# Optimization experiments

Hardware: AMD Instinct MI355X
Metric: run time of the kernel (lower is better)

Reference implementation:

```python
import jax, jax.numpy as jnp
import numpy as np

V_TH = 1.0       # v_threshold
INIT_TAU = 2.0   # raw tau; decay = sigmoid(INIT_TAU)
T, B, IN_SZ, OUT_SZ = 32, 128, 2048, 2048


def setup_inputs() -> dict:
    key = jax.random.key(0)
    k1, k2 = jax.random.split(key)
    x = jax.random.normal(k1, (T, B, IN_SZ), jnp.float32)
    kernel = jax.random.normal(k2, (IN_SZ, OUT_SZ), jnp.float32) / np.sqrt(IN_SZ)
    return {"x": x, "kernel": kernel}


def reference(x, kernel):
    """Forward of Approx_OTPE's inner SNN step (f), scanned over time and
    vmapped over batch. Cell: u' = sigmoid(init_tau)*u + x @ W;
    s = heaviside(u' - v_th); soft reset u_out = u' - s*v_th.
    Returns stacked spikes [T, B, OUT_SZ]."""
    sig_tau = jax.nn.sigmoid(jnp.asarray(INIT_TAU, x.dtype))
    _, batch, _ = x.shape
    out_sz = kernel.shape[1]
    u0 = jnp.zeros((batch, out_sz), x.dtype)

    def body(u, xt):
        u_next = sig_tau * u + xt @ kernel          # [B, O]
        s = (u_next >= V_TH).astype(x.dtype)        # spike_fn forward
        u_out = u_next - s * V_TH                   # soft reset
        return u_out, s

    _, spikes = jax.lax.scan(body, u0, x)
    return spikes
```

## Files before the change

kernel.cpp:

```cpp
#include <hip/hip_runtime.h>
#include <math.h>

constexpr int T_STEPS = 32;
constexpr int BATCH   = 128;
constexpr int IN_SZ   = 2048;
constexpr int OUT_SZ  = 2048;

__global__ __launch_bounds__(256, 1) void Approx_OTPE_67181878444197_kernel(
        const float* __restrict__ x,
        const float* __restrict__ W,
        float* __restrict__ out) {
    constexpr int BK = 32, BM = 128, BN = 64;
    constexpr int YSTR = BN + 1;
    constexpr int YSZ  = BM * YSTR;

    __shared__ float smem[YSZ];
    float* const As = smem;
    float* const Bs = smem + BK * BM;

    const int o0  = blockIdx.x * BN;
    const int b0  = blockIdx.y * 4;
    const int tid = threadIdx.x;
    const int ty  = tid >> 4;
    const int tx  = tid & 15;

    const int am = tid >> 1;
    const int ak = (tid & 1) * 16;
    const int at = am >> 2;
    const int ab = am & 3;
    const size_t aBase = ((size_t)at * BATCH + (size_t)(b0 + ab)) * IN_SZ + ak;

    const int br = tid >> 4;
    const int bc = (tid & 15) * 4;

    float acc[8][4] = {};
    float su[8][4]  = {};

    #pragma unroll 1
    for (int it = 0; it < IN_SZ / BK; ++it) {
        const int k0 = it * BK;
        const float4 a0 = *reinterpret_cast<const float4*>(&x[aBase + k0]);
        const float4 a1 = *reinterpret_cast<const float4*>(&x[aBase + k0 + 4]);
        const float4 a2 = *reinterpret_cast<const float4*>(&x[aBase + k0 + 8]);
        const float4 a3 = *reinterpret_cast<const float4*>(&x[aBase + k0 + 12]);
        const float4 v0 = *reinterpret_cast<const float4*>(
            &W[(size_t)(k0 + br) * OUT_SZ + o0 + bc]);
        const float4 v1 = *reinterpret_cast<const float4*>(
            &W[(size_t)(k0 + 16 + br) * OUT_SZ + o0 + bc]);

        if (it == 16 || it == 32 || it == 48) {
            #pragma unroll
            for (int i = 0; i < 8; ++i)
                #pragma unroll
                for (int j = 0; j < 4; ++j) {
                    su[i][j]  = __fadd_rn(su[i][j], acc[i][j]);
                    acc[i][j] = 0.0f;
                }
        }

        __syncthreads();
        As[(ak +  0) * BM + am] = a0.x;
        As[(ak +  1) * BM + am] = a0.y;
        As[(ak +  2) * BM + am] = a0.z;
        As[(ak +  3) * BM + am] = a0.w;
        As[(ak +  4) * BM + am] = a1.x;
        As[(ak +  5) * BM + am] = a1.y;
        As[(ak +  6) * BM + am] = a1.z;
        As[(ak +  7) * BM + am] = a1.w;
        As[(ak +  8) * BM + am] = a2.x;
        As[(ak +  9) * BM + am] = a2.y;
        As[(ak + 10) * BM + am] = a2.z;
        As[(ak + 11) * BM + am] = a2.w;
        As[(ak + 12) * BM + am] = a3.x;
        As[(ak + 13) * BM + am] = a3.y;
        As[(ak + 14) * BM + am] = a3.z;
        As[(ak + 15) * BM + am] = a3.w;
        *reinterpret_cast<float4*>(&Bs[br * BN + bc])        = v0;
        *reinterpret_cast<float4*>(&Bs[(br + 16) * BN + bc]) = v1;
        __syncthreads();

        #pragma unroll
        for (int k = 0; k < BK; ++k) {
            const float4 x0 = *reinterpret_cast<const float4*>(&As[k * BM + ty * 8]);
            const float4 x1 = *reinterpret_cast<const float4*>(&As[k * BM + ty * 8 + 4]);
            const float4 wf = *reinterpret_cast<const float4*>(&Bs[k * BN + tx * 4]);
            const float a[8] = {x0.x, x0.y, x0.z, x0.w, x1.x, x1.y, x1.z, x1.w};
            const float w[4] = {wf.x, wf.y, wf.z, wf.w};
            #pragma unroll
            for (int i = 0; i < 8; ++i)
                #pragma unroll
                for (int j = 0; j < 4; ++j)
                    acc[i][j] = __builtin_fmaf(a[i], w[j], acc[i][j]);
        }
    }

    __syncthreads();
    #pragma unroll
    for (int i = 0; i < 8; ++i)
        #pragma unroll
        for (int j = 0; j < 4; ++j)
            smem[(ty * 8 + i) * YSTR + tx * 4 + j] = __fadd_rn(su[i][j], acc[i][j]);
    __syncthreads();

    {
        const int bl = tid >> 6;
        const int o  = tid & 63;
        const size_t plane  = (size_t)BATCH * OUT_SZ;
        const size_t outIdx = (size_t)(b0 + bl) * OUT_SZ + o0 + o;

        const double D = 1.0 / (1.0 + exp(-2.0));
        double u = 0.0;
        #pragma unroll
        for (int t = 0; t < T_STEPS; ++t) {
            const double y  = (double)smem[(t * 4 + bl) * YSTR + o];
            const double un = __dadd_rn(__dmul_rn(D, u), y);
            const double s  = (un >= 1.0) ? 1.0 : 0.0;
            u = __dsub_rn(un, s);
            out[(size_t)t * plane + outIdx] = (float)s;
        }
    }
}

extern "C" void kernel_launch(void* const* d_in, const int* in_sizes, int n_in,
                              void* d_out, int out_size, void* d_ws, size_t ws_size,
                              hipStream_t stream) {
    const float* x = (const float*)d_in[0];
    const float* W = (const float*)d_in[1];
    float* out     = (float*)d_out;

    dim3 grid(OUT_SZ / 64, BATCH / 4);
    Approx_OTPE_67181878444197_kernel<<<grid, 256, 0, stream>>>(x, W, out);
}
```

Before: 464.2 us.

## Split-K GEMM into workspace partials then combine and scan in separate kernel

The fused GEMM+scan kernel is replaced, when workspace allows, by a split-K GEMM that writes four partial products over the full T*B row range into a workspace, followed by a kernel that sums the partials in fixed order and runs the spiking scan per (b,o). This gives four times more blocks and a contiguous M tiling to raise occupancy across CUs. In exchange it adds about 128 MB of workspace writes and reads plus a second launch. If the workspace is too small, the original fused kernel is kept as a fallback.

After: 435.3 us. 6.2% less time.

```diff
diff --git a/kernel.cpp b/kernel.cpp
--- a/kernel.cpp
+++ b/kernel.cpp
@@ -5,58 +5,46 @@
 constexpr int BATCH   = 128;
 constexpr int IN_SZ   = 2048;
 constexpr int OUT_SZ  = 2048;
+constexpr int M_ROWS  = T_STEPS * BATCH;
+
 
 __global__ __launch_bounds__(256, 1) void Approx_OTPE_67181878444197_kernel(
         const float* __restrict__ x,
         const float* __restrict__ W,
-        float* __restrict__ out) {
+        float* __restrict__ ws) {
     constexpr int BK = 32, BM = 128, BN = 64;
-    constexpr int YSTR = BN + 1;
-    constexpr int YSZ  = BM * YSTR;
-
-    __shared__ float smem[YSZ];
-    float* const As = smem;
-    float* const Bs = smem + BK * BM;
+
+    __shared__ float As[BK * BM];
+    __shared__ float Bs[BK * BN];
 
     const int o0  = blockIdx.x * BN;
-    const int b0  = blockIdx.y * 4;
+    const int m0  = blockIdx.y * BM;
+    const int z   = blockIdx.z;
+    const int kz  = z * 512;
     const int tid = threadIdx.x;
     const int ty  = tid >> 4;
     const int tx  = tid & 15;
 
     const int am = tid >> 1;
     const int ak = (tid & 1) * 16;
-    const int at = am >> 2;
-    const int ab = am & 3;
-    const size_t aBase = ((size_t)at * BATCH + (size_t)(b0 + ab)) * IN_SZ + ak;
+    const size_t aBase = (size_t)(m0 + am) * IN_SZ + kz + ak;
 
     const int br = tid >> 4;
     const int bc = (tid & 15) * 4;
 
     float acc[8][4] = {};
-    float su[8][4]  = {};
 
     #pragma unroll 1
-    for (int it = 0; it < IN_SZ / BK; ++it) {
+    for (int it = 0; it < 512 / BK; ++it) {
         const int k0 = it * BK;
         const float4 a0 = *reinterpret_cast<const float4*>(&x[aBase + k0]);
         const float4 a1 = *reinterpret_cast<const float4*>(&x[aBase + k0 + 4]);
         const float4 a2 = *reinterpret_cast<const float4*>(&x[aBase + k0 + 8]);
         const float4 a3 = *reinterpret_cast<const float4*>(&x[aBase + k0 + 12]);
         const float4 v0 = *reinterpret_cast<const float4*>(
-            &W[(size_t)(k0 + br) * OUT_SZ + o0 + bc]);
+            &W[(size_t)(kz + k0 + br) * OUT_SZ + o0 + bc]);
         const float4 v1 = *reinterpret_cast<const float4*>(
-            &W[(size_t)(k0 + 16 + br) * OUT_SZ + o0 + bc]);
-
-        if (it == 16 || it == 32 || it == 48) {
-            #pragma unroll
-            for (int i = 0; i < 8; ++i)
-                #pragma unroll
-                for (int j = 0; j < 4; ++j) {
-                    su[i][j]  = __fadd_rn(su[i][j], acc[i][j]);
-                    acc[i][j] = 0.0f;
-                }
-        }
+            &W[(size_t)(kz + k0 + 16 + br) * OUT_SZ + o0 + bc]);
 
         __syncthreads();
         As[(ak +  0) * BM + am] = a0.x;
@@ -94,6 +82,132 @@
         }
     }
 
+    float* const wz = ws + (size_t)z * M_ROWS * OUT_SZ;
+    #pragma unroll
+    for (int i = 0; i < 8; ++i) {
+        float4 v;
+        v.x = acc[i][0]; v.y = acc[i][1]; v.z = acc[i][2]; v.w = acc[i][3];
+        *reinterpret_cast<float4*>(
+            &wz[(size_t)(m0 + ty * 8 + i) * OUT_SZ + o0 + tx * 4]) = v;
+    }
+}
+
+__global__ __launch_bounds__(256, 1) void snn_combine_scan(
+        const float* __restrict__ ws, float* __restrict__ out) {
+    const int gid = blockIdx.x * 256 + threadIdx.x;
+    const int b   = gid >> 11;
+    const int o   = gid & 2047;
+    const size_t plane = (size_t)BATCH * OUT_SZ;
+    constexpr size_t ZS = (size_t)M_ROWS * OUT_SZ;
+
+    const double D = 1.0 / (1.0 + exp(-2.0));
+    double u = 0.0;
+    #pragma unroll 1
+    for (int t = 0; t < T_STEPS; ++t) {
+        const size_t r = (size_t)(t * BATCH + b) * OUT_SZ + o;
+        const float p0 = ws[r];
+        const float p1 = ws[r + ZS];
+        const float p2 = ws[r + 2 * ZS];
+        const float p3 = ws[r + 3 * ZS];
+        float y = __fadd_rn(0.0f, p0);
+        y = __fadd_rn(y, p1);
+        y = __fadd_rn(y, p2);
+        y = __fadd_rn(y, p3);
+        const double un = __dadd_rn(__dmul_rn(D, u), (double)y);
+        const double s  = (un >= 1.0) ? 1.0 : 0.0;
+        u = __dsub_rn(un, s);
+        out[(size_t)t * plane + gid] = (float)s;
+    }
+}
+
+__global__ __launch_bounds__(256, 1) void snn_fused_r25(
+        const float* __restrict__ x,
+        const float* __restrict__ W,
+        float* __restrict__ out) {
+    constexpr int BK = 32, BM = 128, BN = 64;
+    constexpr int YSTR = BN + 1;
+    constexpr int YSZ  = BM * YSTR;
+
+    __shared__ float smem[YSZ];
+    float* const As = smem;
+    float* const Bs = smem + BK * BM;
+
+    const int o0  = blockIdx.x * BN;
+    const int b0  = blockIdx.y * 4;
+    const int tid = threadIdx.x;
+    const int ty  = tid >> 4;
+    const int tx  = tid & 15;
+
+    const int am = tid >> 1;
+    const int ak = (tid & 1) * 16;
+    const int at = am >> 2;
+    const int ab = am & 3;
+    const size_t aBase = ((size_t)at * BATCH + (size_t)(b0 + ab)) * IN_SZ + ak;
+
+    const int br = tid >> 4;
+    const int bc = (tid & 15) * 4;
+
+    float acc[8][4] = {};
+    float su[8][4]  = {};
+
+    #pragma unroll 1
+    for (int it = 0; it < IN_SZ / BK; ++it) {
+        const int k0 = it * BK;
+        const float4 a0 = *reinterpret_cast<const float4*>(&x[aBase + k0]);
+        const float4 a1 = *reinterpret_cast<const float4*>(&x[aBase + k0 + 4]);
+        const float4 a2 = *reinterpret_cast<const float4*>(&x[aBase + k0 + 8]);
+        const float4 a3 = *reinterpret_cast<const float4*>(&x[aBase + k0 + 12]);
+        const float4 v0 = *reinterpret_cast<const float4*>(
+            &W[(size_t)(k0 + br) * OUT_SZ + o0 + bc]);
+        const float4 v1 = *reinterpret_cast<const float4*>(
+            &W[(size_t)(k0 + 16 + br) * OUT_SZ + o0 + bc]);
+
+        if (it == 16 || it == 32 || it == 48) {
+            #pragma unroll
+            for (int i = 0; i < 8; ++i)
+                #pragma unroll
+                for (int j = 0; j < 4; ++j) {
+                    su[i][j]  = __fadd_rn(su[i][j], acc[i][j]);
+                    acc[i][j] = 0.0f;
+                }
+        }
+
+        __syncthreads();
+        As[(ak +  0) * BM + am] = a0.x;
+        As[(ak +  1) * BM + am] = a0.y;
+        As[(ak +  2) * BM + am] = a0.z;
+        As[(ak +  3) * BM + am] = a0.w;
+        As[(ak +  4) * BM + am] = a1.x;
+        As[(ak +  5) * BM + am] = a1.y;
+        As[(ak +  6) * BM + am] = a1.z;
+        As[(ak +  7) * BM + am] = a1.w;
+        As[(ak +  8) * BM + am] = a2.x;
+        As[(ak +  9) * BM + am] = a2.y;
+        As[(ak + 10) * BM + am] = a2.z;
+        As[(ak + 11) * BM + am] = a2.w;
+        As[(ak + 12) * BM + am] = a3.x;
+        As[(ak + 13) * BM + am] = a3.y;
+        As[(ak + 14) * BM + am] = a3.z;
+        As[(ak + 15) * BM + am] = a3.w;
+        *reinterpret_cast<float4*>(&Bs[br * BN + bc])        = v0;
+        *reinterpret_cast<float4*>(&Bs[(br + 16) * BN + bc]) = v1;
+        __syncthreads();
+
+        #pragma unroll
+        for (int k = 0; k < BK; ++k) {
+            const float4 x0 = *reinterpret_cast<const float4*>(&As[k * BM + ty * 8]);
+            const float4 x1 = *reinterpret_cast<const float4*>(&As[k * BM + ty * 8 + 4]);
+            const float4 wf = *reinterpret_cast<const float4*>(&Bs[k * BN + tx * 4]);
+            const float a[8] = {x0.x, x0.y, x0.z, x0.w, x1.x, x1.y, x1.z, x1.w};
+            const float w[4] = {wf.x, wf.y, wf.z, wf.w};
+            #pragma unroll
+            for (int i = 0; i < 8; ++i)
+                #pragma unroll
+                for (int j = 0; j < 4; ++j)
+                    acc[i][j] = __builtin_fmaf(a[i], w[j], acc[i][j]);
+        }
+    }
+
     __syncthreads();
     #pragma unroll
     for (int i = 0; i < 8; ++i)
@@ -128,6 +242,15 @@
     const float* W = (const float*)d_in[1];
     float* out     = (float*)d_out;
 
-    dim3 grid(OUT_SZ / 64, BATCH / 4);
-    Approx_OTPE_67181878444197_kernel<<<grid, 256, 0, stream>>>(x, W, out);
-}
+    const size_t wsNeeded = (size_t)4 * M_ROWS * OUT_SZ * sizeof(float);
+    if (ws_size >= wsNeeded) {
+        dim3 g1(OUT_SZ / 64, M_ROWS / 128, 4);
+        Approx_OTPE_67181878444197_kernel<<<g1, 256, 0, stream>>>(
+            x, W, (float*)d_ws);
+        snn_combine_scan<<<(BATCH * OUT_SZ) / 256, 256, 0, stream>>>(
+            (const float*)d_ws, out);
+    } else {
+        dim3 grid(OUT_SZ / 64, BATCH / 4);
+        snn_fused_r25<<<grid, 256, 0, stream>>>(x, W, out);
+    }
+}
```
